# Kernel optimization log

Hardware: AMD Instinct MI355X
Metric: run time of the kernel (lower is better)

## Reference

```python
import jax, jax.numpy as jnp
import numpy as np

N_NODES = 50000
N_EDGES = 600000
D = 128        # input_dim == hidden_dim
OUT = 2        # output_dim
N_LAYERS = 6


def setup_inputs() -> dict:
    key = jax.random.key(0)
    ks = jax.random.split(key, 6)
    scale = 1.0 / np.sqrt(D)
    x = jax.random.normal(ks[0], (N_NODES, D), jnp.float32)
    edge_index = jax.random.randint(ks[1], (2, N_EDGES), 0, N_NODES)
    Wl = jax.random.normal(ks[2], (N_LAYERS, D, D), jnp.float32) * scale  # neighbor (lin_l) weights
    Wr = jax.random.normal(ks[3], (N_LAYERS, D, D), jnp.float32) * scale  # root (lin_r) weights
    bl = jnp.zeros((N_LAYERS, D), jnp.float32)                            # lin_l bias
    fc_W = jax.random.normal(ks[4], (D, OUT), jnp.float32) * scale
    fc_b = jnp.zeros((OUT,), jnp.float32)
    return {"x": x, "edge_index": edge_index, "Wl": Wl, "Wr": Wr, "bl": bl,
            "fc_W": fc_W, "fc_b": fc_b}


def _sage_conv(h, src, dst, deg_inv, Wl_i, Wr_i, bl_i):
    # mean aggregation over incoming edges: gather -> scatter-add -> normalize
    agg = jax.ops.segment_sum(h[src], dst, num_segments=h.shape[0]) * deg_inv  # [N, D]
    return agg @ Wl_i + h @ Wr_i + bl_i


def reference(x, edge_index, Wl, Wr, bl, fc_W, fc_b):
    src, dst = edge_index[0], edge_index[1]
    deg = jax.ops.segment_sum(jnp.ones(src.shape, x.dtype), dst, num_segments=x.shape[0])
    deg_inv = (1.0 / jnp.maximum(deg, 1.0))[:, None]  # [N, 1]
    h = x
    # ReLU follows every SAGEConv: inner act of each GraphSAGE block + explicit F.relu after each block
    for i in range(N_LAYERS):
        h = _sage_conv(h, src, dst, deg_inv, Wl[i], Wr[i], bl[i])
        h = jax.nn.relu(h)
    return h @ fc_W + fc_b  # [N, OUT]
```

## Files before the change

### kernel.cpp

```cpp
#include <hip/hip_runtime.h>
#include <hip/hip_bf16.h>

#define N_NODES 50000
#define N_EDGES 600000
#define DD 128
#define N_LAYERS 6
#define SCAN_BLOCKS 196

typedef __attribute__((ext_vector_type(8))) short bf16x8;
typedef __attribute__((ext_vector_type(4))) float floatx4;

__device__ __forceinline__ void ldsdma16(const void* g, void* l) {
    __builtin_amdgcn_global_load_lds(
        (const __attribute__((address_space(1))) char*)g,
        (__attribute__((address_space(3))) char*)l, 16, 0, 0);
}

__device__ __forceinline__ unsigned short f2b(float f) {
    unsigned u = __float_as_uint(f);
    unsigned r = (u + 0x7FFFu + ((u >> 16) & 1u)) >> 16;
    return (unsigned short)r;
}


__global__ void zero_counts(int* __restrict__ deg, int* __restrict__ cursor) {
    int i = blockIdx.x * blockDim.x + threadIdx.x;
    if (i < N_NODES) { deg[i] = 0; cursor[i] = 0; }
}

__global__ void count_deg(const int* __restrict__ dst, int* __restrict__ deg) {
    int e = blockIdx.x * blockDim.x + threadIdx.x;
    if (e < N_EDGES) atomicAdd(&deg[dst[e]], 1);
}

__global__ void block_sums(const int* __restrict__ deg, int* __restrict__ bsum) {
    __shared__ int s[256];
    int tid = threadIdx.x;
    int i = blockIdx.x * 256 + tid;
    int v = (i < N_NODES) ? deg[i] : 0;
    s[tid] = v;
    __syncthreads();
    #pragma unroll
    for (int off = 128; off > 0; off >>= 1) {
        if (tid < off) s[tid] += s[tid + off];
        __syncthreads();
    }
    if (tid == 0) bsum[blockIdx.x] = s[0];
}

__global__ void scan_bsums(int* __restrict__ bsum, int* __restrict__ offsets) {
    __shared__ int s[256];
    int tid = threadIdx.x;
    int v = (tid < SCAN_BLOCKS) ? bsum[tid] : 0;
    s[tid] = v;
    __syncthreads();
    for (int off = 1; off < 256; off <<= 1) {
        int t = (tid >= off) ? s[tid - off] : 0;
        __syncthreads();
        s[tid] += t;
        __syncthreads();
    }
    if (tid < SCAN_BLOCKS) bsum[tid] = s[tid] - v;
    if (tid == 0) offsets[N_NODES] = N_EDGES;
}

__global__ void write_offsets(const int* __restrict__ deg, const int* __restrict__ bsum,
                              int* __restrict__ offsets, float* __restrict__ deg_inv) {
    __shared__ int s[256];
    int tid = threadIdx.x;
    int i = blockIdx.x * 256 + tid;
    int v = (i < N_NODES) ? deg[i] : 0;
    s[tid] = v;
    __syncthreads();
    for (int off = 1; off < 256; off <<= 1) {
        int t = (tid >= off) ? s[tid - off] : 0;
        __syncthreads();
        s[tid] += t;
        __syncthreads();
    }
    if (i < N_NODES) {
        offsets[i] = bsum[blockIdx.x] + s[tid] - v;
        deg_inv[i] = 1.0f / (float)(v > 1 ? v : 1);
    }
}

__global__ void fill_csr(const int* __restrict__ src, const int* __restrict__ dst,
                         const int* __restrict__ offsets, int* __restrict__ cursor,
                         int* __restrict__ csr_src) {
    int e = blockIdx.x * blockDim.x + threadIdx.x;
    if (e < N_EDGES) {
        int d = dst[e];
        int p = atomicAdd(&cursor[d], 1);
        csr_src[offsets[d] + p] = src[e];
    }
}


__global__ void x_to_bf16(const float* __restrict__ x, unsigned short* __restrict__ hx) {
    int idx = blockIdx.x * blockDim.x + threadIdx.x;
    int b = idx * 4;
    float4 v = *(const float4*)(x + b);
    ushort4 o;
    o.x = f2b(v.x); o.y = f2b(v.y); o.z = f2b(v.z); o.w = f2b(v.w);
    *(ushort4*)(hx + b) = o;
}

__global__ void prep_weights(const float* __restrict__ Wl, const float* __restrict__ Wr,
                             unsigned short* __restrict__ WT2) {
    int idx = blockIdx.x * blockDim.x + threadIdx.x;
    int l   = idx >> 15;
    int rem = idx & 32767;
    int n   = rem >> 8;
    int k2  = rem & 255;
    const float* W = (k2 < 128 ? Wl : Wr) + (size_t)l * DD * DD + (size_t)(k2 & 127) * DD + n;
    WT2[idx] = f2b(*W);
}


__global__ void aggregate(const unsigned short* __restrict__ hin, const int* __restrict__ offsets,
                          const int* __restrict__ csr_src, const float* __restrict__ deg_inv,
                          unsigned short* __restrict__ agg) {
    int wid  = threadIdx.x >> 6;
    int lane = threadIdx.x & 63;
    int grp  = lane >> 4;
    int l16  = lane & 15;
    int node = blockIdx.x * 4 + wid;
    if (node >= N_NODES) return;
    int s = offsets[node], e = offsets[node + 1];

    float a0=0,a1=0,a2=0,a3=0,a4=0,a5=0,a6=0,a7=0;
    for (int j = s + grp; j < e; j += 4) {
        int src = csr_src[j];
        uint4 v = *(const uint4*)(hin + (size_t)src * DD + l16 * 8);
        a0 += __uint_as_float(v.x << 16); a1 += __uint_as_float(v.x & 0xFFFF0000u);
        a2 += __uint_as_float(v.y << 16); a3 += __uint_as_float(v.y & 0xFFFF0000u);
        a4 += __uint_as_float(v.z << 16); a5 += __uint_as_float(v.z & 0xFFFF0000u);
        a6 += __uint_as_float(v.w << 16); a7 += __uint_as_float(v.w & 0xFFFF0000u);
    }
    a0 += __shfl_xor(a0, 16, 64); a1 += __shfl_xor(a1, 16, 64);
    a2 += __shfl_xor(a2, 16, 64); a3 += __shfl_xor(a3, 16, 64);
    a4 += __shfl_xor(a4, 16, 64); a5 += __shfl_xor(a5, 16, 64);
    a6 += __shfl_xor(a6, 16, 64); a7 += __shfl_xor(a7, 16, 64);
    a0 += __shfl_xor(a0, 32, 64); a1 += __shfl_xor(a1, 32, 64);
    a2 += __shfl_xor(a2, 32, 64); a3 += __shfl_xor(a3, 32, 64);
    a4 += __shfl_xor(a4, 32, 64); a5 += __shfl_xor(a5, 32, 64);
    a6 += __shfl_xor(a6, 32, 64); a7 += __shfl_xor(a7, 32, 64);

    if (grp == 0) {
        float di = deg_inv[node];
        uint4 o;
        o.x = (unsigned)f2b(a0 * di) | ((unsigned)f2b(a1 * di) << 16);
        o.y = (unsigned)f2b(a2 * di) | ((unsigned)f2b(a3 * di) << 16);
        o.z = (unsigned)f2b(a4 * di) | ((unsigned)f2b(a5 * di) << 16);
        o.w = (unsigned)f2b(a6 * di) | ((unsigned)f2b(a7 * di) << 16);
        *(uint4*)(agg + (size_t)node * DD + l16 * 8) = o;
    }
}


__launch_bounds__(256)
__global__ void gemm_mfma(const unsigned short* __restrict__ Agg,
                          const unsigned short* __restrict__ H,
                          const unsigned short* __restrict__ WT2,
                          const float* __restrict__ bias,
                          unsigned short* __restrict__ Cout) {
    __shared__ unsigned short sA[128 * 32];
    __shared__ unsigned short sW[128 * 32];

    int tid  = threadIdx.x;
    int lane = tid & 63, wid = tid >> 6;
    int wm = wid >> 1, wn = wid & 1;
    int n0 = blockIdx.x * 128;

    floatx4 acc[4][4];
    #pragma unroll
    for (int i = 0; i < 4; ++i)
        #pragma unroll
        for (int j = 0; j < 4; ++j)
            acc[i][j] = (floatx4){0.f, 0.f, 0.f, 0.f};

    int c0 = tid, c1 = tid + 256;
    int rA0 = c0 >> 2, qA0 = (c0 & 3) ^ ((rA0 >> 1) & 3);
    int rA1 = c1 >> 2, qA1 = (c1 & 3) ^ ((rA1 >> 1) & 3);
    int gr0 = n0 + rA0; if (gr0 > N_NODES - 1) gr0 = N_NODES - 1;
    int gr1 = n0 + rA1; if (gr1 > N_NODES - 1) gr1 = N_NODES - 1;

    int l15 = lane & 15, q = lane >> 4;

    #pragma unroll
    for (int half = 0; half < 2; ++half) {
        const unsigned short* X = half ? H : Agg;
        #pragma unroll
        for (int kk = 0; kk < 4; ++kk) {
            int k0 = kk * 32;
            int k2 = half * 128 + k0;
            ldsdma16(X + (size_t)gr0 * DD + k0 + qA0 * 8, sA + c0 * 8);
            ldsdma16(X + (size_t)gr1 * DD + k0 + qA1 * 8, sA + c1 * 8);
            ldsdma16(WT2 + (size_t)rA0 * 256 + k2 + qA0 * 8, sW + c0 * 8);
            ldsdma16(WT2 + (size_t)rA1 * 256 + k2 + qA1 * 8, sW + c1 * 8);
            __syncthreads();

            bf16x8 aF[4], bF[4];
            #pragma unroll
            for (int i = 0; i < 4; ++i) {
                int row = wm * 64 + i * 16 + l15;
                int ca  = row * 4 + (q ^ ((row >> 1) & 3));
                aF[i] = *(const bf16x8*)(sA + ca * 8);
                int nn = wn * 64 + i * 16 + l15;
                int cb = nn * 4 + (q ^ ((nn >> 1) & 3));
                bF[i] = *(const bf16x8*)(sW + cb * 8);
            }
            #pragma unroll
            for (int i = 0; i < 4; ++i)
                #pragma unroll
                for (int j = 0; j < 4; ++j)
                    acc[i][j] = __builtin_amdgcn_mfma_f32_16x16x32_bf16(aF[i], bF[j], acc[i][j], 0, 0, 0);
            __syncthreads();
        }
    }

    float bcol[4];
    #pragma unroll
    for (int j = 0; j < 4; ++j) bcol[j] = bias[wn * 64 + j * 16 + l15];
    #pragma unroll
    for (int i = 0; i < 4; ++i) {
        #pragma unroll
        for (int r = 0; r < 4; ++r) {
            int row = n0 + wm * 64 + i * 16 + q * 4 + r;
            if (row < N_NODES) {
                #pragma unroll
                for (int j = 0; j < 4; ++j) {
                    int col = wn * 64 + j * 16 + l15;
                    float v = acc[i][j][r] + bcol[j];
                    v = fmaxf(v, 0.f);
                    Cout[(size_t)row * DD + col] = f2b(v);
                }
            }
        }
    }
}


__global__ void fc_kernel(const unsigned short* __restrict__ h, const float* __restrict__ fcW,
                          const float* __restrict__ fcb, float* __restrict__ out) {
    int n = blockIdx.x * blockDim.x + threadIdx.x;
    if (n >= N_NODES) return;
    const unsigned* hr = (const unsigned*)(h + (size_t)n * DD);
    float s0 = fcb[0], s1 = fcb[1];
    #pragma unroll 8
    for (int k = 0; k < 64; ++k) {
        unsigned v = hr[k];
        float h0 = __uint_as_float(v << 16);
        float h1 = __uint_as_float(v & 0xFFFF0000u);
        s0 += h0 * fcW[(2 * k) * 2]     + h1 * fcW[(2 * k + 1) * 2];
        s1 += h0 * fcW[(2 * k) * 2 + 1] + h1 * fcW[(2 * k + 1) * 2 + 1];
    }
    out[n * 2] = s0; out[n * 2 + 1] = s1;
}


extern "C" void kernel_launch(void* const* d_in, const int* in_sizes, int n_in,
                              void* d_out, int out_size, void* d_ws, size_t ws_size,
                              hipStream_t stream) {
    const float* x    = (const float*)d_in[0];
    const int*   ei   = (const int*)d_in[1];
    const float* Wl   = (const float*)d_in[2];
    const float* Wr   = (const float*)d_in[3];
    const float* bl   = (const float*)d_in[4];
    const float* fcW  = (const float*)d_in[5];
    const float* fcb  = (const float*)d_in[6];
    float* out = (float*)d_out;

    const int* srcIdx = ei;
    const int* dstIdx = ei + N_EDGES;

    char* ws = (char*)d_ws;
    size_t off = 0;
    auto bump = [&](size_t bytes) { char* p = ws + off; off = (off + bytes + 255) & ~(size_t)255; return p; };
    int*   deg     = (int*)  bump(N_NODES * 4);
    int*   cursor  = (int*)  bump(N_NODES * 4);
    int*   offsets = (int*)  bump((N_NODES + 1) * 4);
    int*   bsum    = (int*)  bump(SCAN_BLOCKS * 4);
    float* deg_inv = (float*)bump(N_NODES * 4);
    int*   csr     = (int*)  bump(N_EDGES * 4);
    unsigned short* hx   = (unsigned short*)bump((size_t)N_NODES * DD * 2);
    unsigned short* hb0  = (unsigned short*)bump((size_t)N_NODES * DD * 2);
    unsigned short* hb1  = (unsigned short*)bump((size_t)N_NODES * DD * 2);
    unsigned short* agg  = (unsigned short*)bump((size_t)N_NODES * DD * 2);
    unsigned short* WT2  = (unsigned short*)bump((size_t)N_LAYERS * 128 * 256 * 2);
    (void)ws_size;

    zero_counts<<<(N_NODES + 255) / 256, 256, 0, stream>>>(deg, cursor);
    count_deg<<<(N_EDGES + 255) / 256, 256, 0, stream>>>(dstIdx, deg);
    block_sums<<<SCAN_BLOCKS, 256, 0, stream>>>(deg, bsum);
    scan_bsums<<<1, 256, 0, stream>>>(bsum, offsets);
    write_offsets<<<SCAN_BLOCKS, 256, 0, stream>>>(deg, bsum, offsets, deg_inv);
    fill_csr<<<(N_EDGES + 255) / 256, 256, 0, stream>>>(srcIdx, dstIdx, offsets, cursor, csr);
    x_to_bf16<<<(N_NODES * DD / 4 + 255) / 256, 256, 0, stream>>>(x, hx);
    prep_weights<<<(N_LAYERS * 128 * 256 + 255) / 256, 256, 0, stream>>>(Wl, Wr, WT2);

    const unsigned short* hin = hx;
    unsigned short* hbuf[2] = { hb0, hb1 };
    for (int l = 0; l < N_LAYERS; ++l) {
        aggregate<<<(N_NODES + 3) / 4, 256, 0, stream>>>(hin, offsets, csr, deg_inv, agg);
        unsigned short* hout = hbuf[l & 1];
        gemm_mfma<<<(N_NODES + 127) / 128, 256, 0, stream>>>(
            agg, hin, WT2 + (size_t)l * 128 * 256, bl + (size_t)l * DD, hout);
        hin = hout;
    }
    fc_kernel<<<(N_NODES + 255) / 256, 256, 0, stream>>>(hin, fcW, fcb, out);
}
```

Baseline: 402.3 us.

## Fuse neighbor aggregation into the per-layer MFMA GEMM via shared memory

Merges the aggregate and gemm kernels into one sage_layer kernel. Each 64-node block gathers and mean-reduces neighbor features into an LDS tile, then multiplies it directly with the weights, so the bf16 agg buffer never goes through global memory and one launch per layer disappears. Each 16-lane group now walks a node's whole edge list serially, with no cross-group split, which gives less memory-level parallelism per node. The GEMM tile shrinks to 64 rows, so weight tiles are reloaded more often and per-node degree imbalance stalls whole blocks.

```diff
diff --git a/kernel.cpp b/kernel.cpp
--- a/kernel.cpp
+++ b/kernel.cpp
@@ -117,101 +117,95 @@
 }
 
 
-__global__ void aggregate(const unsigned short* __restrict__ hin, const int* __restrict__ offsets,
-                          const int* __restrict__ csr_src, const float* __restrict__ deg_inv,
-                          unsigned short* __restrict__ agg) {
-    int wid  = threadIdx.x >> 6;
-    int lane = threadIdx.x & 63;
-    int grp  = lane >> 4;
-    int l16  = lane & 15;
-    int node = blockIdx.x * 4 + wid;
-    if (node >= N_NODES) return;
-    int s = offsets[node], e = offsets[node + 1];
-
-    float a0=0,a1=0,a2=0,a3=0,a4=0,a5=0,a6=0,a7=0;
-    for (int j = s + grp; j < e; j += 4) {
-        int src = csr_src[j];
-        uint4 v = *(const uint4*)(hin + (size_t)src * DD + l16 * 8);
-        a0 += __uint_as_float(v.x << 16); a1 += __uint_as_float(v.x & 0xFFFF0000u);
-        a2 += __uint_as_float(v.y << 16); a3 += __uint_as_float(v.y & 0xFFFF0000u);
-        a4 += __uint_as_float(v.z << 16); a5 += __uint_as_float(v.z & 0xFFFF0000u);
-        a6 += __uint_as_float(v.w << 16); a7 += __uint_as_float(v.w & 0xFFFF0000u);
-    }
-    a0 += __shfl_xor(a0, 16, 64); a1 += __shfl_xor(a1, 16, 64);
-    a2 += __shfl_xor(a2, 16, 64); a3 += __shfl_xor(a3, 16, 64);
-    a4 += __shfl_xor(a4, 16, 64); a5 += __shfl_xor(a5, 16, 64);
-    a6 += __shfl_xor(a6, 16, 64); a7 += __shfl_xor(a7, 16, 64);
-    a0 += __shfl_xor(a0, 32, 64); a1 += __shfl_xor(a1, 32, 64);
-    a2 += __shfl_xor(a2, 32, 64); a3 += __shfl_xor(a3, 32, 64);
-    a4 += __shfl_xor(a4, 32, 64); a5 += __shfl_xor(a5, 32, 64);
-    a6 += __shfl_xor(a6, 32, 64); a7 += __shfl_xor(a7, 32, 64);
-
-    if (grp == 0) {
-        float di = deg_inv[node];
+__launch_bounds__(256)
+__global__ void sage_layer(const unsigned short* __restrict__ H,
+                           const int* __restrict__ offsets,
+                           const int* __restrict__ csr_src,
+                           const float* __restrict__ deg_inv,
+                           const unsigned short* __restrict__ WT2,
+                           const float* __restrict__ bias,
+                           unsigned short* __restrict__ Cout) {
+    __shared__ __align__(16) unsigned short sAgg[64][136];
+    __shared__ __align__(16) unsigned short sA[64 * 32];
+    __shared__ __align__(16) unsigned short sW[128 * 32];
+
+    int tid  = threadIdx.x;
+    int lane = tid & 63, wid = tid >> 6;
+    int n0 = blockIdx.x * 64;
+    int grp = lane >> 4;
+    int l16 = lane & 15;
+
+    #pragma unroll
+    for (int t = 0; t < 4; ++t) {
+        int lrow = wid * 16 + t * 4 + grp;
+        int node = n0 + lrow;
+        int nc = node < N_NODES ? node : N_NODES - 1;
+        int s = offsets[nc], e = offsets[nc + 1];
+        float a0=0,a1=0,a2=0,a3=0,a4=0,a5=0,a6=0,a7=0;
+        for (int j = s; j < e; ++j) {
+            int src = csr_src[j];
+            uint4 v = *(const uint4*)(H + (size_t)src * DD + l16 * 8);
+            a0 += __uint_as_float(v.x << 16); a1 += __uint_as_float(v.x & 0xFFFF0000u);
+            a2 += __uint_as_float(v.y << 16); a3 += __uint_as_float(v.y & 0xFFFF0000u);
+            a4 += __uint_as_float(v.z << 16); a5 += __uint_as_float(v.z & 0xFFFF0000u);
+            a6 += __uint_as_float(v.w << 16); a7 += __uint_as_float(v.w & 0xFFFF0000u);
+        }
+        float di = deg_inv[nc];
         uint4 o;
         o.x = (unsigned)f2b(a0 * di) | ((unsigned)f2b(a1 * di) << 16);
         o.y = (unsigned)f2b(a2 * di) | ((unsigned)f2b(a3 * di) << 16);
         o.z = (unsigned)f2b(a4 * di) | ((unsigned)f2b(a5 * di) << 16);
         o.w = (unsigned)f2b(a6 * di) | ((unsigned)f2b(a7 * di) << 16);
-        *(uint4*)(agg + (size_t)node * DD + l16 * 8) = o;
-    }
-}
-
-
-__launch_bounds__(256)
-__global__ void gemm_mfma(const unsigned short* __restrict__ Agg,
-                          const unsigned short* __restrict__ H,
-                          const unsigned short* __restrict__ WT2,
-                          const float* __restrict__ bias,
-                          unsigned short* __restrict__ Cout) {
-    __shared__ unsigned short sA[128 * 32];
-    __shared__ unsigned short sW[128 * 32];
-
-    int tid  = threadIdx.x;
-    int lane = tid & 63, wid = tid >> 6;
+        *(uint4*)&sAgg[lrow][l16 * 8] = o;
+    }
+    __syncthreads();
+
     int wm = wid >> 1, wn = wid & 1;
-    int n0 = blockIdx.x * 128;
-
-    floatx4 acc[4][4];
-    #pragma unroll
-    for (int i = 0; i < 4; ++i)
+    int l15 = lane & 15, q = lane >> 4;
+
+    floatx4 acc[2][4];
+    #pragma unroll
+    for (int i = 0; i < 2; ++i)
         #pragma unroll
         for (int j = 0; j < 4; ++j)
             acc[i][j] = (floatx4){0.f, 0.f, 0.f, 0.f};
 
-    int c0 = tid, c1 = tid + 256;
-    int rA0 = c0 >> 2, qA0 = (c0 & 3) ^ ((rA0 >> 1) & 3);
-    int rA1 = c1 >> 2, qA1 = (c1 & 3) ^ ((rA1 >> 1) & 3);
-    int gr0 = n0 + rA0; if (gr0 > N_NODES - 1) gr0 = N_NODES - 1;
-    int gr1 = n0 + rA1; if (gr1 > N_NODES - 1) gr1 = N_NODES - 1;
-
-    int l15 = lane & 15, q = lane >> 4;
+    int rA = tid >> 2, qA = (tid & 3) ^ ((rA >> 1) & 3);
+    int grA = n0 + rA; if (grA > N_NODES - 1) grA = N_NODES - 1;
+    int cW1 = tid + 256;
+    int rW0 = tid >> 2, qW0 = (tid & 3) ^ ((rW0 >> 1) & 3);
+    int rW1 = cW1 >> 2, qW1 = (cW1 & 3) ^ ((rW1 >> 1) & 3);
 
     #pragma unroll
     for (int half = 0; half < 2; ++half) {
-        const unsigned short* X = half ? H : Agg;
         #pragma unroll
         for (int kk = 0; kk < 4; ++kk) {
-            int k0 = kk * 32;
-            int k2 = half * 128 + k0;
-            ldsdma16(X + (size_t)gr0 * DD + k0 + qA0 * 8, sA + c0 * 8);
-            ldsdma16(X + (size_t)gr1 * DD + k0 + qA1 * 8, sA + c1 * 8);
-            ldsdma16(WT2 + (size_t)rA0 * 256 + k2 + qA0 * 8, sW + c0 * 8);
-            ldsdma16(WT2 + (size_t)rA1 * 256 + k2 + qA1 * 8, sW + c1 * 8);
+            int k2 = half * 128 + kk * 32;
+            if (half)
+                ldsdma16(H + (size_t)grA * DD + kk * 32 + qA * 8, sA + tid * 8);
+            ldsdma16(WT2 + (size_t)rW0 * 256 + k2 + qW0 * 8, sW + tid * 8);
+            ldsdma16(WT2 + (size_t)rW1 * 256 + k2 + qW1 * 8, sW + cW1 * 8);
             __syncthreads();
 
-            bf16x8 aF[4], bF[4];
+            bf16x8 aF[2], bF[4];
             #pragma unroll
-            for (int i = 0; i < 4; ++i) {
-                int row = wm * 64 + i * 16 + l15;
-                int ca  = row * 4 + (q ^ ((row >> 1) & 3));
-                aF[i] = *(const bf16x8*)(sA + ca * 8);
-                int nn = wn * 64 + i * 16 + l15;
-                int cb = nn * 4 + (q ^ ((nn >> 1) & 3));
-                bF[i] = *(const bf16x8*)(sW + cb * 8);
+            for (int i = 0; i < 2; ++i) {
+                int row = wm * 32 + i * 16 + l15;
+                if (half == 0) {
+                    aF[i] = *(const bf16x8*)&sAgg[row][kk * 32 + q * 8];
+                } else {
+                    int ca = row * 4 + (q ^ ((row >> 1) & 3));
+                    aF[i] = *(const bf16x8*)(sA + ca * 8);
+                }
             }
             #pragma unroll
-            for (int i = 0; i < 4; ++i)
+            for (int j = 0; j < 4; ++j) {
+                int nn = wn * 64 + j * 16 + l15;
+                int cb = nn * 4 + (q ^ ((nn >> 1) & 3));
+                bF[j] = *(const bf16x8*)(sW + cb * 8);
+            }
+            #pragma unroll
+            for (int i = 0; i < 2; ++i)
                 #pragma unroll
                 for (int j = 0; j < 4; ++j)
                     acc[i][j] = __builtin_amdgcn_mfma_f32_16x16x32_bf16(aF[i], bF[j], acc[i][j], 0, 0, 0);
@@ -223,17 +217,16 @@
     #pragma unroll
     for (int j = 0; j < 4; ++j) bcol[j] = bias[wn * 64 + j * 16 + l15];
     #pragma unroll
-    for (int i = 0; i < 4; ++i) {
+    for (int i = 0; i < 2; ++i) {
         #pragma unroll
         for (int r = 0; r < 4; ++r) {
-            int row = n0 + wm * 64 + i * 16 + q * 4 + r;
+            int row = n0 + wm * 32 + i * 16 + q * 4 + r;
             if (row < N_NODES) {
                 #pragma unroll
                 for (int j = 0; j < 4; ++j) {
                     int col = wn * 64 + j * 16 + l15;
                     float v = acc[i][j][r] + bcol[j];
-                    v = fmaxf(v, 0.f);
-                    Cout[(size_t)row * DD + col] = f2b(v);
+                    Cout[(size_t)row * DD + col] = f2b(fmaxf(v, 0.f));
                 }
             }
         }
@@ -286,7 +279,6 @@
     unsigned short* hx   = (unsigned short*)bump((size_t)N_NODES * DD * 2);
     unsigned short* hb0  = (unsigned short*)bump((size_t)N_NODES * DD * 2);
     unsigned short* hb1  = (unsigned short*)bump((size_t)N_NODES * DD * 2);
-    unsigned short* agg  = (unsigned short*)bump((size_t)N_NODES * DD * 2);
     unsigned short* WT2  = (unsigned short*)bump((size_t)N_LAYERS * 128 * 256 * 2);
     (void)ws_size;
 
@@ -302,10 +294,9 @@
     const unsigned short* hin = hx;
     unsigned short* hbuf[2] = { hb0, hb1 };
     for (int l = 0; l < N_LAYERS; ++l) {
-        aggregate<<<(N_NODES + 3) / 4, 256, 0, stream>>>(hin, offsets, csr, deg_inv, agg);
         unsigned short* hout = hbuf[l & 1];
-        gemm_mfma<<<(N_NODES + 127) / 128, 256, 0, stream>>>(
-            agg, hin, WT2 + (size_t)l * 128 * 256, bl + (size_t)l * DD, hout);
+        sage_layer<<<(N_NODES + 63) / 64, 256, 0, stream>>>(
+            hin, offsets, csr, deg_inv, WT2 + (size_t)l * 128 * 256, bl + (size_t)l * DD, hout);
         hin = hout;
     }
     fc_kernel<<<(N_NODES + 255) / 256, 256, 0, stream>>>(hin, fcW, fcb, out);
```

After: 491.1 us. 22.1% more time.

## Keep layer weights resident in LDS with persistent per-wave 16-row GEMM chunks

Applied to the files above, without the earlier changes.

Replaces the tiled 128x128 GEMM, which reloaded weight slices for every K step with block-wide barriers, with a persistent kernel. Each block loads the full 128x256 bf16 weight matrix into LDS once. Each wave then loops over 16-row chunks, loading its own A tile via LDS DMA and running 8x8 MFMAs without block synchronisation. This removes redundant weight traffic and barrier stalls. The cost is about 128KB of LDS per block, which limits occupancy, plus a serialized load-then-compute loop per wave with no prefetch.

```diff
diff --git a/kernel.cpp b/kernel.cpp
--- a/kernel.cpp
+++ b/kernel.cpp
@@ -6,6 +6,7 @@
 #define DD 128
 #define N_LAYERS 6
 #define SCAN_BLOCKS 196
+#define N_CHUNKS 3125
 
 typedef __attribute__((ext_vector_type(8))) short bf16x8;
 typedef __attribute__((ext_vector_type(4))) float floatx4;
@@ -158,83 +159,74 @@
 }
 
 
-__launch_bounds__(256)
-__global__ void gemm_mfma(const unsigned short* __restrict__ Agg,
+__launch_bounds__(512, 2)
+__global__ void gemm_resW(const unsigned short* __restrict__ Agg,
                           const unsigned short* __restrict__ H,
                           const unsigned short* __restrict__ WT2,
                           const float* __restrict__ bias,
                           unsigned short* __restrict__ Cout) {
-    __shared__ unsigned short sA[128 * 32];
-    __shared__ unsigned short sW[128 * 32];
+    __shared__ __align__(16) unsigned short sW[128 * 256];
+    __shared__ __align__(16) unsigned short sA[8][4096];
 
     int tid  = threadIdx.x;
-    int lane = tid & 63, wid = tid >> 6;
-    int wm = wid >> 1, wn = wid & 1;
-    int n0 = blockIdx.x * 128;
-
-    floatx4 acc[4][4];
+    int wid  = tid >> 6, lane = tid & 63;
+    int l15  = lane & 15, q = lane >> 4;
+
+    for (int t = tid; t < 4096; t += 512) {
+        int col = t >> 5, c = t & 31;
+        uint4 v = *(const uint4*)(WT2 + (size_t)col * 256 + c * 8);
+        *(uint4*)(sW + ((size_t)col * 32 + (c ^ (col & 7))) * 8) = v;
+    }
+    __syncthreads();
+
+    float bcol[8];
     #pragma unroll
-    for (int i = 0; i < 4; ++i)
-        #pragma unroll
-        for (int j = 0; j < 4; ++j)
-            acc[i][j] = (floatx4){0.f, 0.f, 0.f, 0.f};
-
-    int c0 = tid, c1 = tid + 256;
-    int rA0 = c0 >> 2, qA0 = (c0 & 3) ^ ((rA0 >> 1) & 3);
-    int rA1 = c1 >> 2, qA1 = (c1 & 3) ^ ((rA1 >> 1) & 3);
-    int gr0 = n0 + rA0; if (gr0 > N_NODES - 1) gr0 = N_NODES - 1;
-    int gr1 = n0 + rA1; if (gr1 > N_NODES - 1) gr1 = N_NODES - 1;
-
-    int l15 = lane & 15, q = lane >> 4;
-
-    #pragma unroll
-    for (int half = 0; half < 2; ++half) {
-        const unsigned short* X = half ? H : Agg;
-        #pragma unroll
-        for (int kk = 0; kk < 4; ++kk) {
-            int k0 = kk * 32;
-            int k2 = half * 128 + k0;
-            ldsdma16(X + (size_t)gr0 * DD + k0 + qA0 * 8, sA + c0 * 8);
-            ldsdma16(X + (size_t)gr1 * DD + k0 + qA1 * 8, sA + c1 * 8);
-            ldsdma16(WT2 + (size_t)rA0 * 256 + k2 + qA0 * 8, sW + c0 * 8);
-            ldsdma16(WT2 + (size_t)rA1 * 256 + k2 + qA1 * 8, sW + c1 * 8);
-            __syncthreads();
-
-            bf16x8 aF[4], bF[4];
+    for (int j = 0; j < 8; ++j) bcol[j] = bias[j * 16 + l15];
+
+    unsigned short* myA = &sA[wid][0];
+
+    for (int chunk = blockIdx.x * 8 + wid; chunk < N_CHUNKS; chunk += 2048) {
+        int row0 = chunk * 16;
+        #pragma unroll
+        for (int i = 0; i < 4; ++i) {
+            int r  = i * 4 + q;
+            int cg = l15 ^ (r & 7);
+            ldsdma16(Agg + (size_t)(row0 + r) * DD + cg * 8, myA + (size_t)i * 512 + lane * 8);
+        }
+        #pragma unroll
+        for (int i = 0; i < 4; ++i) {
+            int r  = i * 4 + q;
+            int cg = l15 ^ (r & 7);
+            ldsdma16(H + (size_t)(row0 + r) * DD + cg * 8, myA + 2048 + (size_t)i * 512 + lane * 8);
+        }
+        __builtin_amdgcn_s_waitcnt(0);
+
+        floatx4 acc[8];
+        #pragma unroll
+        for (int j = 0; j < 8; ++j) acc[j] = (floatx4){0.f, 0.f, 0.f, 0.f};
+
+        #pragma unroll
+        for (int s = 0; s < 8; ++s) {
+            int cglob = s * 4 + q;
+            int reg   = cglob >> 4;
+            int cin   = cglob & 15;
+            bf16x8 aF = *(const bf16x8*)(myA + (size_t)reg * 2048 +
+                                         ((size_t)l15 * 16 + (cin ^ (l15 & 7))) * 8);
             #pragma unroll
-            for (int i = 0; i < 4; ++i) {
-                int row = wm * 64 + i * 16 + l15;
-                int ca  = row * 4 + (q ^ ((row >> 1) & 3));
-                aF[i] = *(const bf16x8*)(sA + ca * 8);
-                int nn = wn * 64 + i * 16 + l15;
-                int cb = nn * 4 + (q ^ ((nn >> 1) & 3));
-                bF[i] = *(const bf16x8*)(sW + cb * 8);
+            for (int j = 0; j < 8; ++j) {
+                int col = j * 16 + l15;
+                bf16x8 bF = *(const bf16x8*)(sW + ((size_t)col * 32 + (cglob ^ (col & 7))) * 8);
+                acc[j] = __builtin_amdgcn_mfma_f32_16x16x32_bf16(aF, bF, acc[j], 0, 0, 0);
             }
+        }
+
+        #pragma unroll
+        for (int r = 0; r < 4; ++r) {
+            int row = row0 + q * 4 + r;
             #pragma unroll
-            for (int i = 0; i < 4; ++i)
-                #pragma unroll
-                for (int j = 0; j < 4; ++j)
-                    acc[i][j] = __builtin_amdgcn_mfma_f32_16x16x32_bf16(aF[i], bF[j], acc[i][j], 0, 0, 0);
-            __syncthreads();
-        }
-    }
-
-    float bcol[4];
-    #pragma unroll
-    for (int j = 0; j < 4; ++j) bcol[j] = bias[wn * 64 + j * 16 + l15];
-    #pragma unroll
-    for (int i = 0; i < 4; ++i) {
-        #pragma unroll
-        for (int r = 0; r < 4; ++r) {
-            int row = n0 + wm * 64 + i * 16 + q * 4 + r;
-            if (row < N_NODES) {
-                #pragma unroll
-                for (int j = 0; j < 4; ++j) {
-                    int col = wn * 64 + j * 16 + l15;
-                    float v = acc[i][j][r] + bcol[j];
-                    v = fmaxf(v, 0.f);
-                    Cout[(size_t)row * DD + col] = f2b(v);
-                }
+            for (int j = 0; j < 8; ++j) {
+                float v = acc[j][r] + bcol[j];
+                Cout[(size_t)row * DD + j * 16 + l15] = f2b(fmaxf(v, 0.f));
             }
         }
     }
@@ -304,7 +296,7 @@
     for (int l = 0; l < N_LAYERS; ++l) {
         aggregate<<<(N_NODES + 3) / 4, 256, 0, stream>>>(hin, offsets, csr, deg_inv, agg);
         unsigned short* hout = hbuf[l & 1];
-        gemm_mfma<<<(N_NODES + 127) / 128, 256, 0, stream>>>(
+        gemm_resW<<<256, 512, 0, stream>>>(
             agg, hin, WT2 + (size_t)l * 128 * 256, bl + (size_t)l * DD, hout);
         hin = hout;
     }
```

New measurement: 401.7 us. Within noise of the previous version (-0.1%).
